# Kernel tuning notes

Hardware: AMD Instinct MI355X
Metric: run time of the kernel (lower is better)

Reference implementation:

```python
import jax, jax.numpy as jnp
import numpy as np

B, T, V, E, H, L = 64, 512, 256, 1024, 1024, 2


def setup_inputs() -> dict:
    key = jax.random.key(0)
    ks = jax.random.split(key, 9)
    s = 1.0 / np.sqrt(H)
    X = jax.random.randint(ks[0], (B, T), 0, V)
    h0 = jax.random.uniform(ks[1], (L, B, H), dtype=jnp.float32)
    emb = (jax.random.normal(ks[2], (V, E), dtype=jnp.float32) * 0.02).at[0].set(0.0)  # pad_idx=0 row zeroed
    W_ih = jax.random.normal(ks[3], (L, 3 * H, H), dtype=jnp.float32) * s
    W_hh = jax.random.normal(ks[4], (L, 3 * H, H), dtype=jnp.float32) * s
    b_ih = jax.random.normal(ks[5], (L, 3 * H), dtype=jnp.float32) * s
    b_hh = jax.random.normal(ks[6], (L, 3 * H), dtype=jnp.float32) * s
    W_out = jax.random.normal(ks[7], (V, H), dtype=jnp.float32) * s
    b_out = jax.random.normal(ks[8], (V,), dtype=jnp.float32) * s
    return {"X": X, "h0": h0, "emb": emb, "W_ih": W_ih, "W_hh": W_hh,
            "b_ih": b_ih, "b_hh": b_hh, "W_out": W_out, "b_out": b_out}


def _gru_layer(x, h0_l, W_ih_l, W_hh_l, b_ih_l, b_hh_l):
    # x: [B, T, D]; PyTorch GRU cell math (gate order r, z, n).
    gx = jnp.einsum('btd,gd->btg', x, W_ih_l) + b_ih_l  # [B, T, 3H], precomputed input GEMM

    def step(h, gx_t):  # gx_t: [B, 3H]
        gh = h @ W_hh_l.T + b_hh_l
        xr, xz, xn = jnp.split(gx_t, 3, axis=-1)
        hr, hz, hn = jnp.split(gh, 3, axis=-1)
        r = jax.nn.sigmoid(xr + hr)
        z = jax.nn.sigmoid(xz + hz)
        n = jnp.tanh(xn + r * hn)
        h_new = (1.0 - z) * n + z * h
        return h_new, h_new

    _, ys = jax.lax.scan(step, h0_l, jnp.swapaxes(gx, 0, 1))  # scan over time
    return jnp.swapaxes(ys, 0, 1)  # [B, T, H]


def reference(X, h0, emb, W_ih, W_hh, b_ih, b_hh, W_out, b_out):
    # Embedding lookup (dropout is identity in eval mode)
    x = emb[X]  # [B, T, E]
    for l in range(L):
        x = _gru_layer(x, h0[l], W_ih[l], W_hh[l], b_ih[l], b_hh[l])
    logits = jnp.einsum('bth,vh->btv', x, W_out) + b_out  # [B, T, V]
    # fptt returns out[:, :-1].reshape(-1, token_count)
    return logits[:, :-1, :].reshape(-1, V)
```

## Files before the change

kernel.cpp:

```cpp
#include <hip/hip_runtime.h>
#include <stdint.h>


namespace {

constexpr int B = 64, T = 512, V = 256, H = 1024, G = 3072;
constexpr int NBLK = 192;

typedef _Float16 f16;
typedef unsigned long long u64;
typedef f16 f16x8 __attribute__((ext_vector_type(8)));
typedef f16 f16x4 __attribute__((ext_vector_type(4)));
typedef float f32x4 __attribute__((ext_vector_type(4)));

#define MFMA16(av, bv, acc) __builtin_amdgcn_mfma_f32_16x16x32_f16(av, bv, acc, 0, 0, 0)

__device__ __forceinline__ f16x8 aload16(const f16* p) {
  u64 lo = __hip_atomic_load(reinterpret_cast<const u64*>(p), __ATOMIC_RELAXED,
                             __HIP_MEMORY_SCOPE_AGENT);
  u64 hi = __hip_atomic_load(reinterpret_cast<const u64*>(p) + 1,
                             __ATOMIC_RELAXED, __HIP_MEMORY_SCOPE_AGENT);
  union { u64 q[2]; f16x8 v; } u;
  u.q[0] = lo; u.q[1] = hi;
  return u.v;
}
__device__ __forceinline__ float aload2(const f16* p) {
  unsigned short s = __hip_atomic_load(
      reinterpret_cast<const unsigned short*>(p), __ATOMIC_RELAXED,
      __HIP_MEMORY_SCOPE_AGENT);
  union { unsigned short s; f16 f; } u;
  u.s = s;
  return (float)u.f;
}
__device__ __forceinline__ void astore2(f16* p, float v) {
  union { f16 f; unsigned short s; } u;
  u.f = (f16)v;
  __hip_atomic_store(reinterpret_cast<unsigned short*>(p), u.s,
                     __ATOMIC_RELAXED, __HIP_MEMORY_SCOPE_AGENT);
}
__device__ __forceinline__ float aloadf(const float* p) {
  return __hip_atomic_load(p, __ATOMIC_RELAXED, __HIP_MEMORY_SCOPE_AGENT);
}
__device__ __forceinline__ void astoref(float* p, float v) {
  __hip_atomic_store(p, v, __ATOMIC_RELAXED, __HIP_MEMORY_SCOPE_AGENT);
}
__device__ __forceinline__ void astorei(int* p, int v) {
  __hip_atomic_store(p, v, __ATOMIC_RELAXED, __HIP_MEMORY_SCOPE_AGENT);
}

__device__ __forceinline__ void poll3(const int* p0, const int* p1,
                                      const int* p2, int& a0, int& a1,
                                      int& a2) {
  asm volatile(
      "global_load_dword %0, %3, off sc1\n\t"
      "global_load_dword %1, %4, off sc1\n\t"
      "global_load_dword %2, %5, off sc1\n\t"
      "s_waitcnt vmcnt(0)"
      : "=&v"(a0), "=&v"(a1), "=&v"(a2)
      : "v"(p0), "v"(p1), "v"(p2)
      : "memory");
}

__device__ __forceinline__ void mm48(const f16* a, const f16* wp, f32x4& aR,
                                     f32x4& aZ, f32x4& aN) {
  f16x8 ring[8];
#pragma unroll
  for (int q = 0; q < 8; ++q) ring[q] = aload16(a + q * 2048);
#pragma unroll
  for (int k0 = 0; k0 < 32; ++k0) {
    f16x8 av = ring[k0 & 7];
    if (k0 + 8 < 32) ring[k0 & 7] = aload16(a + (k0 + 8) * 2048);
    const f16* w = wp + k0 * 1728;
    aR = MFMA16(av, *reinterpret_cast<const f16x8*>(w), aR);
    aZ = MFMA16(av, *reinterpret_cast<const f16x8*>(w + 576), aZ);
    aN = MFMA16(av, *reinterpret_cast<const f16x8*>(w + 1152), aN);
  }
}

__global__ void to_f16_4(const float* __restrict__ src, f16* __restrict__ dst,
                         int n4) {
  int i = blockIdx.x * 256 + threadIdx.x;
  if (i >= n4) return;
  float4 v = reinterpret_cast<const float4*>(src)[i];
  f16x4 o = {(f16)v.x, (f16)v.y, (f16)v.z, (f16)v.w};
  reinterpret_cast<f16x4*>(dst)[i] = o;
}

__global__ void pack_w(const float* __restrict__ Whh,
                       const float* __restrict__ Wih, f16* __restrict__ dst) {
  const int id = blockIdx.x * 256 + threadIdx.x;
  const int kkq = id & 3;
  const int rr = id >> 2;
  const int row = rr % 48;
  const int rest = rr / 48;
  const int k0 = rest & 31, bi = (rest >> 5) & 63, which = rest >> 11;
  const int g = row >> 4, jrow = row & 15;
  const float* base = (which == 0) ? Whh
                    : (which == 1) ? (Wih + (size_t)G * H)
                                   : (Whh + (size_t)G * H);
  const float* src =
      base + ((size_t)(g * H + bi * 16 + jrow)) * H + k0 * 32 + kkq * 8;
  float4 a = *reinterpret_cast<const float4*>(src);
  float4 b = *reinterpret_cast<const float4*>(src + 4);
  f16x8 o = {(f16)a.x, (f16)a.y, (f16)a.z, (f16)a.w,
             (f16)b.x, (f16)b.y, (f16)b.z, (f16)b.w};
  *reinterpret_cast<f16x8*>(dst + (size_t)id * 8) = o;
}

__global__ void pack_h0f(const float* __restrict__ h0, f16* __restrict__ h1,
                         f16* __restrict__ h2, int* __restrict__ bar) {
  if (blockIdx.x == 0 && threadIdx.x < NBLK) {
    bar[threadIdx.x * 16] = 0;
    bar[4096 + threadIdx.x * 16] = 0;
  }
  const int id = blockIdx.x * 256 + threadIdx.x;
  const int layer = id >> 16, b = (id >> 10) & 63, j = id & 1023;
  const size_t a = ((size_t)(j >> 5) * 64 + b) * 32 + (j & 31);
  const f16 v = (f16)h0[id];
  if (layer == 0) h1[a] = v; else h2[a] = v;
}

template <int MODE>
__global__ __launch_bounds__(256) void gemm_f16(
    const f16* __restrict__ A, const f16* __restrict__ Bm,
    const float* __restrict__ bias, float* __restrict__ C, int M, int N,
    int K) {
  __shared__ __align__(16) f16 As[64][48], Bs[64][48];

  const int tid = threadIdx.x;
  const int lane = tid & 63, wv = tid >> 6;
  const int bm = blockIdx.y, bn = blockIdx.x;
  const int srow = tid >> 2, sseg = (tid & 3) * 8;

  const f16* pA = (MODE == 2)
                      ? (A + (size_t)bm * 65536 + srow * 32 + sseg)
                      : (A + (size_t)(bm * 64 + srow) * K + sseg);
  const f16* pB = Bm + (size_t)(bn * 64 + srow) * K + sseg;

  f32x4 acc[4];
  const f32x4 zero = {0.f, 0.f, 0.f, 0.f};
#pragma unroll
  for (int nt = 0; nt < 4; ++nt) acc[nt] = zero;

  const int ar = wv * 16 + (lane & 15);
  const int kk = (lane >> 4) * 8;

  const int niter = K / 32;
  for (int ki = 0; ki < niter; ++ki) {
    int4 va = (MODE == 2) ? *reinterpret_cast<const int4*>(pA + ki * 2048)
                          : *reinterpret_cast<const int4*>(pA + ki * 32);
    int4 vb = *reinterpret_cast<const int4*>(pB + ki * 32);
    __syncthreads();
    *reinterpret_cast<int4*>(&As[srow][sseg]) = va;
    *reinterpret_cast<int4*>(&Bs[srow][sseg]) = vb;
    __syncthreads();

    f16x8 av = *reinterpret_cast<const f16x8*>(&As[ar][kk]);
#pragma unroll
    for (int nt = 0; nt < 4; ++nt) {
      f16x8 bv = *reinterpret_cast<const f16x8*>(&Bs[nt * 16 + (lane & 15)][kk]);
      acc[nt] = MFMA16(av, bv, acc[nt]);
    }
  }

  const int rbase = wv * 16 + (lane >> 4) * 4;
  const int cl = lane & 15;
#pragma unroll
  for (int nt = 0; nt < 4; ++nt) {
    const int n = bn * 64 + nt * 16 + cl;
    const float bv = bias[n];
#pragma unroll
    for (int r = 0; r < 4; ++r) {
      const int m = bm * 64 + rbase + r;
      const float v = acc[nt][r] + bv;
      if (MODE == 0) {
        C[(size_t)m * N + n] = v;
      } else {
        const int t = m >> 6, bb = m & 63;
        if (t < T - 1) C[((size_t)(bb * (T - 1) + t)) * V + n] = v;
      }
    }
  }
}

__global__ __launch_bounds__(256, 1) void gru_persist(
    const f16* __restrict__ pW, const float* __restrict__ G0,
    const int* __restrict__ X, const float* __restrict__ b_hh,
    const float* __restrict__ b_ih, f16* __restrict__ h1a,
    f16* __restrict__ h1b, f16* __restrict__ h2a, f16* __restrict__ h2b,
    float* __restrict__ gx2, f16* __restrict__ y2, int* __restrict__ bar) {
  __shared__ __align__(16) f16 Wt[55296];

  const int tid = threadIdx.x, bx = blockIdx.x;
  const int lane = tid & 63, wv = tid >> 6;
  const int l15 = lane & 15, kq = lane >> 4;
  const int role = bx >> 6, jb = bx & 63;

  int* arrive = bar;
  int* door = bar + 4096;

  {
    const int2* src = reinterpret_cast<const int2*>(pW + (size_t)bx * 49152);
#pragma unroll
    for (int q = 0; q < 48; ++q) {
      const int flat = q * 256 + tid;
      const int k0r = flat >> 3, seg = flat & 7;
      *reinterpret_cast<int2*>(&Wt[k0r * 36 + seg * 4]) = src[flat];
    }
  }
  __syncthreads();

  const int j = jb * 16 + l15;
  float br_ = 0.f, bz_ = 0.f, bn_ = 0.f, bxr_ = 0.f, bxz_ = 0.f, bxn_ = 0.f;
  if (role == 0) {
    br_ = b_hh[j]; bz_ = b_hh[H + j]; bn_ = b_hh[2 * H + j];
  } else if (role == 2) {
    br_ = b_hh[G + j]; bz_ = b_hh[G + H + j]; bn_ = b_hh[G + 2 * H + j];
    bxr_ = b_ih[G + j]; bxz_ = b_ih[G + H + j]; bxn_ = b_ih[G + 2 * H + j];
  }

  f16* h1buf[2] = {h1a, h1b};
  f16* h2buf[2] = {h2a, h2b};
  const int aoff = (wv * 16 + l15) * 32 + kq * 8;
  const f16* wp = Wt + l15 * 36 + kq * 8;
  const int bB = wv * 16 + kq * 4;
  const size_t hoff = (size_t)(j >> 5) * 2048 + (j & 31);

  for (int i = 0; i <= T + 1; ++i) {
    if (role == 0) {
      if (i < T) {
        const f16* hin = h1buf[i & 1];
        f16* hout = h1buf[(i + 1) & 1];
        f32x4 aR = {0, 0, 0, 0}, aZ = {0, 0, 0, 0}, aN = {0, 0, 0, 0};
        mm48(hin + aoff, wp, aR, aZ, aN);
#pragma unroll
        for (int r = 0; r < 4; ++r) {
          const int b = bB + r;
          const float* gx = G0 + (size_t)X[b * T + i] * G;
          const float xr = gx[j], xz = gx[H + j], xn = gx[2 * H + j];
          const size_t ha = hoff + (size_t)b * 32;
          const float hp = aload2(hin + ha);
          const float rg = 1.f / (1.f + __expf(-(xr + aR[r] + br_)));
          const float zg = 1.f / (1.f + __expf(-(xz + aZ[r] + bz_)));
          const float ng = tanhf(xn + rg * (aN[r] + bn_));
          astore2(hout + ha, (1.f - zg) * ng + zg * hp);
        }
      }
    } else if (role == 1) {
      if (i >= 1 && i <= T) {
        const int t = i - 1;
        f32x4 aR = {0, 0, 0, 0}, aZ = {0, 0, 0, 0}, aN = {0, 0, 0, 0};
        mm48(h1buf[i & 1] + aoff, wp, aR, aZ, aN);
        float* gdst = gx2 + ((size_t)(t & 1) * 64 + jb) * 3072;
#pragma unroll
        for (int r = 0; r < 4; ++r) {
          const int b = bB + r;
          astoref(gdst + b * 16 + l15, aR[r]);
          astoref(gdst + 1024 + b * 16 + l15, aZ[r]);
          astoref(gdst + 2048 + b * 16 + l15, aN[r]);
        }
      }
    } else {
      if (i >= 2) {
        const int t = i - 2;
        const f16* hin = h2buf[i & 1];
        f16* hout = h2buf[(i + 1) & 1];
        const float* gsrc = gx2 + ((size_t)(t & 1) * 64 + jb) * 3072;
        f32x4 aR = {0, 0, 0, 0}, aZ = {0, 0, 0, 0}, aN = {0, 0, 0, 0};
        mm48(hin + aoff, wp, aR, aZ, aN);
#pragma unroll
        for (int r = 0; r < 4; ++r) {
          const int b = bB + r;
          const float xr = aloadf(gsrc + b * 16 + l15);
          const float xz = aloadf(gsrc + 1024 + b * 16 + l15);
          const float xn = aloadf(gsrc + 2048 + b * 16 + l15);
          const size_t ha = hoff + (size_t)b * 32;
          const float hp = aload2(hin + ha);
          const float rg = 1.f / (1.f + __expf(-(xr + bxr_ + aR[r] + br_)));
          const float zg = 1.f / (1.f + __expf(-(xz + bxz_ + aZ[r] + bz_)));
          const float ng = tanhf(xn + bxn_ + rg * (aN[r] + bn_));
          const float hv = (1.f - zg) * ng + zg * hp;
          astore2(hout + ha, hv);
          y2[(size_t)t * 65536 + ha] = (f16)hv;
        }
      }
    }

    asm volatile("" ::: "memory");
    __syncthreads();
    const int ph = i + 1;
    if (tid == 0) astorei(&arrive[bx * 16], ph);
    if (bx == 0) {
      if (tid < 64) {
        int a0, a1, a2;
        for (;;) {
          poll3(&arrive[tid * 16], &arrive[(64 + tid) * 16],
                &arrive[(128 + tid) * 16], a0, a1, a2);
          if (__all(a0 >= ph && a1 >= ph && a2 >= ph)) break;
          __builtin_amdgcn_s_sleep(1);
        }
        astorei(&door[tid * 16], ph);
        astorei(&door[(64 + tid) * 16], ph);
        astorei(&door[(128 + tid) * 16], ph);
      }
    } else if (tid == 0) {
      while (__hip_atomic_load(&door[bx * 16], __ATOMIC_RELAXED,
                               __HIP_MEMORY_SCOPE_AGENT) < ph) {
        __builtin_amdgcn_s_sleep(1);
      }
    }
    __syncthreads();
    asm volatile("" ::: "memory");
  }
}

}

extern "C" void kernel_launch(void* const* d_in, const int* in_sizes, int n_in,
                              void* d_out, int out_size, void* d_ws,
                              size_t ws_size, hipStream_t stream) {
  const int* X = (const int*)d_in[0];
  const float* h0 = (const float*)d_in[1];
  const float* emb = (const float*)d_in[2];
  const float* W_ih = (const float*)d_in[3];
  const float* W_hh = (const float*)d_in[4];
  const float* b_ih = (const float*)d_in[5];
  const float* b_hh = (const float*)d_in[6];
  const float* W_out = (const float*)d_in[7];
  const float* b_out = (const float*)d_in[8];
  float* out = (float*)d_out;
  (void)in_sizes; (void)n_in; (void)out_size; (void)ws_size;

  char* p = (char*)d_ws;
  auto alloc = [&](size_t bytes) {
    char* q = p;
    p += (bytes + 255) & ~(size_t)255;
    return q;
  };
  f16* pW = (f16*)alloc((size_t)3 * 64 * 49152 * 2);
  float* G0 = (float*)alloc((size_t)V * G * 4);
  f16* emb16 = (f16*)alloc((size_t)V * H * 2);
  f16* wih0_16 = (f16*)alloc((size_t)G * H * 2);
  f16* wout16 = (f16*)alloc((size_t)V * H * 2);
  f16* h1a = (f16*)alloc((size_t)B * H * 2);
  f16* h1b = (f16*)alloc((size_t)B * H * 2);
  f16* h2a = (f16*)alloc((size_t)B * H * 2);
  f16* h2b = (f16*)alloc((size_t)B * H * 2);
  float* gx2 = (float*)alloc((size_t)2 * 64 * 3072 * 4);
  f16* y2 = (f16*)alloc((size_t)T * B * H * 2);
  int* bar = (int*)alloc(32768);

  to_f16_4<<<(V * H / 4 + 255) / 256, 256, 0, stream>>>(emb, emb16, V * H / 4);
  to_f16_4<<<(G * H / 4 + 255) / 256, 256, 0, stream>>>(W_ih, wih0_16,
                                                        G * H / 4);
  to_f16_4<<<(V * H / 4 + 255) / 256, 256, 0, stream>>>(W_out, wout16,
                                                        V * H / 4);
  pack_w<<<4608, 256, 0, stream>>>(W_hh, W_ih, pW);
  pack_h0f<<<512, 256, 0, stream>>>(h0, h1a, h2a, bar);
  gemm_f16<0><<<dim3(G / 64, V / 64), 256, 0, stream>>>(emb16, wih0_16, b_ih,
                                                        G0, V, G, H);

  {
    const f16* a0 = pW; const float* a1 = G0; const int* a2 = X;
    const float* a3 = b_hh; const float* a4 = b_ih;
    f16* a5 = h1a; f16* a6 = h1b; f16* a7 = h2a; f16* a8 = h2b;
    float* a9 = gx2; f16* a10 = y2; int* a11 = bar;
    void* args[] = {&a0, &a1, &a2, &a3, &a4, &a5, &a6,
                    &a7, &a8, &a9, &a10, &a11};
    hipLaunchCooperativeKernel((const void*)gru_persist, dim3(NBLK), dim3(256),
                               args, 0, stream);
  }

  gemm_f16<2><<<dim3(V / 64, T), 256, 0, stream>>>(y2, wout16, b_out, out,
                                                   T * B, V, H);
}
```

Measured before the change: 7.954 ms.

## Replace double-buffered hidden states with ring buffers and plain cached loads

Hidden states move from ping-pong double buffers to a 128-slot ring for layer 1 and a full 513-slot history for layer 2. Because each slot is written only once per phase, reads can use plain vector loads in place of the per-8-byte relaxed atomic loads. The layer-2 history now serves directly as the output-projection input, which drops the separate y2 store. Correctness relies on never reading stale cached lines, so an explicit s_waitcnt vmcnt(0) is added before the barrier, and the larger ring buffers add memory footprint.

```diff
diff --git a/kernel.cpp b/kernel.cpp
--- a/kernel.cpp
+++ b/kernel.cpp
@@ -6,6 +6,8 @@
 
 constexpr int B = 64, T = 512, V = 256, H = 1024, G = 3072;
 constexpr int NBLK = 192;
+constexpr int SLAB = 65536;
+constexpr int R1MASK = 127;
 
 typedef _Float16 f16;
 typedef unsigned long long u64;
@@ -15,23 +17,11 @@
 
 #define MFMA16(av, bv, acc) __builtin_amdgcn_mfma_f32_16x16x32_f16(av, bv, acc, 0, 0, 0)
 
-__device__ __forceinline__ f16x8 aload16(const f16* p) {
-  u64 lo = __hip_atomic_load(reinterpret_cast<const u64*>(p), __ATOMIC_RELAXED,
-                             __HIP_MEMORY_SCOPE_AGENT);
-  u64 hi = __hip_atomic_load(reinterpret_cast<const u64*>(p) + 1,
-                             __ATOMIC_RELAXED, __HIP_MEMORY_SCOPE_AGENT);
-  union { u64 q[2]; f16x8 v; } u;
-  u.q[0] = lo; u.q[1] = hi;
-  return u.v;
-}
-__device__ __forceinline__ float aload2(const f16* p) {
-  unsigned short s = __hip_atomic_load(
-      reinterpret_cast<const unsigned short*>(p), __ATOMIC_RELAXED,
-      __HIP_MEMORY_SCOPE_AGENT);
-  union { unsigned short s; f16 f; } u;
-  u.s = s;
-  return (float)u.f;
-}
+__device__ __forceinline__ f16x8 lload16(const f16* p) {
+  return *reinterpret_cast<const f16x8*>(p);
+}
+__device__ __forceinline__ float lload2(const f16* p) { return (float)*p; }
+
 __device__ __forceinline__ void astore2(f16* p, float v) {
   union { f16 f; unsigned short s; } u;
   u.f = (f16)v;
@@ -65,11 +55,11 @@
                                      f32x4& aZ, f32x4& aN) {
   f16x8 ring[8];
 #pragma unroll
-  for (int q = 0; q < 8; ++q) ring[q] = aload16(a + q * 2048);
+  for (int q = 0; q < 8; ++q) ring[q] = lload16(a + q * 2048);
 #pragma unroll
   for (int k0 = 0; k0 < 32; ++k0) {
     f16x8 av = ring[k0 & 7];
-    if (k0 + 8 < 32) ring[k0 & 7] = aload16(a + (k0 + 8) * 2048);
+    if (k0 + 8 < 32) ring[k0 & 7] = lload16(a + (k0 + 8) * 2048);
     const f16* w = wp + k0 * 1728;
     aR = MFMA16(av, *reinterpret_cast<const f16x8*>(w), aR);
     aZ = MFMA16(av, *reinterpret_cast<const f16x8*>(w + 576), aZ);
@@ -107,8 +97,8 @@
   *reinterpret_cast<f16x8*>(dst + (size_t)id * 8) = o;
 }
 
-__global__ void pack_h0f(const float* __restrict__ h0, f16* __restrict__ h1,
-                         f16* __restrict__ h2, int* __restrict__ bar) {
+__global__ void pack_h0f(const float* __restrict__ h0, f16* __restrict__ h1r,
+                         f16* __restrict__ h2r, int* __restrict__ bar) {
   if (blockIdx.x == 0 && threadIdx.x < NBLK) {
     bar[threadIdx.x * 16] = 0;
     bar[4096 + threadIdx.x * 16] = 0;
@@ -117,7 +107,7 @@
   const int layer = id >> 16, b = (id >> 10) & 63, j = id & 1023;
   const size_t a = ((size_t)(j >> 5) * 64 + b) * 32 + (j & 31);
   const f16 v = (f16)h0[id];
-  if (layer == 0) h1[a] = v; else h2[a] = v;
+  if (layer == 0) h1r[a] = v; else h2r[a] = v;
 }
 
 template <int MODE>
@@ -186,9 +176,8 @@
 __global__ __launch_bounds__(256, 1) void gru_persist(
     const f16* __restrict__ pW, const float* __restrict__ G0,
     const int* __restrict__ X, const float* __restrict__ b_hh,
-    const float* __restrict__ b_ih, f16* __restrict__ h1a,
-    f16* __restrict__ h1b, f16* __restrict__ h2a, f16* __restrict__ h2b,
-    float* __restrict__ gx2, f16* __restrict__ y2, int* __restrict__ bar) {
+    const float* __restrict__ b_ih, f16* __restrict__ h1ring,
+    f16* __restrict__ h2ring, float* __restrict__ gx2, int* __restrict__ bar) {
   __shared__ __align__(16) f16 Wt[55296];
 
   const int tid = threadIdx.x, bx = blockIdx.x;
@@ -219,8 +208,6 @@
     bxr_ = b_ih[G + j]; bxz_ = b_ih[G + H + j]; bxn_ = b_ih[G + 2 * H + j];
   }
 
-  f16* h1buf[2] = {h1a, h1b};
-  f16* h2buf[2] = {h2a, h2b};
   const int aoff = (wv * 16 + l15) * 32 + kq * 8;
   const f16* wp = Wt + l15 * 36 + kq * 8;
   const int bB = wv * 16 + kq * 4;
@@ -229,8 +216,8 @@
   for (int i = 0; i <= T + 1; ++i) {
     if (role == 0) {
       if (i < T) {
-        const f16* hin = h1buf[i & 1];
-        f16* hout = h1buf[(i + 1) & 1];
+        const f16* hin = h1ring + (size_t)(i & R1MASK) * SLAB;
+        f16* hout = h1ring + (size_t)((i + 1) & R1MASK) * SLAB;
         f32x4 aR = {0, 0, 0, 0}, aZ = {0, 0, 0, 0}, aN = {0, 0, 0, 0};
         mm48(hin + aoff, wp, aR, aZ, aN);
 #pragma unroll
@@ -239,7 +226,7 @@
           const float* gx = G0 + (size_t)X[b * T + i] * G;
           const float xr = gx[j], xz = gx[H + j], xn = gx[2 * H + j];
           const size_t ha = hoff + (size_t)b * 32;
-          const float hp = aload2(hin + ha);
+          const float hp = lload2(hin + ha);
           const float rg = 1.f / (1.f + __expf(-(xr + aR[r] + br_)));
           const float zg = 1.f / (1.f + __expf(-(xz + aZ[r] + bz_)));
           const float ng = tanhf(xn + rg * (aN[r] + bn_));
@@ -250,7 +237,7 @@
       if (i >= 1 && i <= T) {
         const int t = i - 1;
         f32x4 aR = {0, 0, 0, 0}, aZ = {0, 0, 0, 0}, aN = {0, 0, 0, 0};
-        mm48(h1buf[i & 1] + aoff, wp, aR, aZ, aN);
+        mm48(h1ring + (size_t)(i & R1MASK) * SLAB + aoff, wp, aR, aZ, aN);
         float* gdst = gx2 + ((size_t)(t & 1) * 64 + jb) * 3072;
 #pragma unroll
         for (int r = 0; r < 4; ++r) {
@@ -263,8 +250,8 @@
     } else {
       if (i >= 2) {
         const int t = i - 2;
-        const f16* hin = h2buf[i & 1];
-        f16* hout = h2buf[(i + 1) & 1];
+        const f16* hin = h2ring + (size_t)t * SLAB;
+        f16* hout = h2ring + (size_t)(t + 1) * SLAB;
         const float* gsrc = gx2 + ((size_t)(t & 1) * 64 + jb) * 3072;
         f32x4 aR = {0, 0, 0, 0}, aZ = {0, 0, 0, 0}, aN = {0, 0, 0, 0};
         mm48(hin + aoff, wp, aR, aZ, aN);
@@ -275,18 +262,18 @@
           const float xz = aloadf(gsrc + 1024 + b * 16 + l15);
           const float xn = aloadf(gsrc + 2048 + b * 16 + l15);
           const size_t ha = hoff + (size_t)b * 32;
-          const float hp = aload2(hin + ha);
+          const float hp = lload2(hin + ha);
           const float rg = 1.f / (1.f + __expf(-(xr + bxr_ + aR[r] + br_)));
           const float zg = 1.f / (1.f + __expf(-(xz + bxz_ + aZ[r] + bz_)));
           const float ng = tanhf(xn + bxn_ + rg * (aN[r] + bn_));
           const float hv = (1.f - zg) * ng + zg * hp;
           astore2(hout + ha, hv);
-          y2[(size_t)t * 65536 + ha] = (f16)hv;
         }
       }
     }
 
-    asm volatile("" ::: "memory");
+    asm volatile("s_waitcnt vmcnt(0)" ::: "memory");
+    __builtin_amdgcn_sched_barrier(0);
     __syncthreads();
     const int ph = i + 1;
     if (tid == 0) astorei(&arrive[bx * 16], ph);
@@ -342,12 +329,9 @@
   f16* emb16 = (f16*)alloc((size_t)V * H * 2);
   f16* wih0_16 = (f16*)alloc((size_t)G * H * 2);
   f16* wout16 = (f16*)alloc((size_t)V * H * 2);
-  f16* h1a = (f16*)alloc((size_t)B * H * 2);
-  f16* h1b = (f16*)alloc((size_t)B * H * 2);
-  f16* h2a = (f16*)alloc((size_t)B * H * 2);
-  f16* h2b = (f16*)alloc((size_t)B * H * 2);
+  f16* h1ring = (f16*)alloc((size_t)128 * 65536 * 2);
+  f16* h2ring = (f16*)alloc((size_t)513 * 65536 * 2);
   float* gx2 = (float*)alloc((size_t)2 * 64 * 3072 * 4);
-  f16* y2 = (f16*)alloc((size_t)T * B * H * 2);
   int* bar = (int*)alloc(32768);
 
   to_f16_4<<<(V * H / 4 + 255) / 256, 256, 0, stream>>>(emb, emb16, V * H / 4);
@@ -356,21 +340,19 @@
   to_f16_4<<<(V * H / 4 + 255) / 256, 256, 0, stream>>>(W_out, wout16,
                                                         V * H / 4);
   pack_w<<<4608, 256, 0, stream>>>(W_hh, W_ih, pW);
-  pack_h0f<<<512, 256, 0, stream>>>(h0, h1a, h2a, bar);
+  pack_h0f<<<512, 256, 0, stream>>>(h0, h1ring, h2ring, bar);
   gemm_f16<0><<<dim3(G / 64, V / 64), 256, 0, stream>>>(emb16, wih0_16, b_ih,
                                                         G0, V, G, H);
 
   {
     const f16* a0 = pW; const float* a1 = G0; const int* a2 = X;
     const float* a3 = b_hh; const float* a4 = b_ih;
-    f16* a5 = h1a; f16* a6 = h1b; f16* a7 = h2a; f16* a8 = h2b;
-    float* a9 = gx2; f16* a10 = y2; int* a11 = bar;
-    void* args[] = {&a0, &a1, &a2, &a3, &a4, &a5, &a6,
-                    &a7, &a8, &a9, &a10, &a11};
+    f16* a5 = h1ring; f16* a6 = h2ring; float* a7 = gx2; int* a8 = bar;
+    void* args[] = {&a0, &a1, &a2, &a3, &a4, &a5, &a6, &a7, &a8};
     hipLaunchCooperativeKernel((const void*)gru_persist, dim3(NBLK), dim3(256),
                                args, 0, stream);
   }
 
-  gemm_f16<2><<<dim3(V / 64, T), 256, 0, stream>>>(y2, wout16, b_out, out,
-                                                   T * B, V, H);
-}
+  gemm_f16<2><<<dim3(V / 64, T), 256, 0, stream>>>(h2ring + 65536, wout16,
+                                                   b_out, out, T * B, V, H);
+}
```

Measured after the change: 7.419 ms. -6.7%, faster.
